# Kernel tuning notes

Measured on AMD Instinct MI355X. Metric: run time of the kernel, lower is better.

Reference implementation:

```python
import jax, jax.numpy as jnp
import numpy as np

N = 50000          # nodes
E = 1_600_000      # edges (avg degree 32)
IN = 16            # in_node_features
H0 = 64            # hidden_features_mlp[0]
D = 32             # hidden_features_mlp[1] == hidden_features_gnn
HF = 64            # hidden_final
OUT = 3            # out_features (congestion classes)
L = 3              # gnn_layer_num
EPS = 1e-5


def gelu(x):
    return jax.nn.gelu(x, approximate=False)  # torch nn.GELU default (erf)


def bn_eval(x, g, b):
    # BatchNorm1d in eval mode with fresh running stats (mean=0, var=1)
    return x * (g / jnp.sqrt(1.0 + EPS)) + b


def ln(x, g, b):
    m = jnp.mean(x, axis=-1, keepdims=True)
    v = jnp.var(x, axis=-1, keepdims=True)
    return (x - m) / jnp.sqrt(v + EPS) * g + b


def setup_inputs() -> dict:
    key = jax.random.key(0)
    ks = jax.random.split(key, 24)
    s = 0.1
    inp = {
        "x": jax.random.normal(ks[0], (N, IN), dtype=jnp.float32),
        "edge_index": jax.random.randint(ks[1], (2, E), 0, N, dtype=jnp.int32),
        # node_emb_mlp
        "emb_W1": jax.random.normal(ks[2], (IN, H0), dtype=jnp.float32) * s,
        "emb_b1": jnp.zeros((H0,), jnp.float32),
        "emb_bn1_g": jnp.ones((H0,), jnp.float32),
        "emb_bn1_b": jnp.zeros((H0,), jnp.float32),
        "emb_W2": jax.random.normal(ks[3], (H0, D), dtype=jnp.float32) * s,
        "emb_b2": jnp.zeros((D,), jnp.float32),
        "emb_bn2_g": jnp.ones((D,), jnp.float32),
        "emb_bn2_b": jnp.zeros((D,), jnp.float32),
        # GNN layers (stacked over L)
        "msg_W": jax.random.normal(ks[4], (L, 2 * D, D), dtype=jnp.float32) * s,
        "msg_b": jnp.zeros((L, D), jnp.float32),
        "msg_ln_g": jnp.ones((L, D), jnp.float32),
        "msg_ln_b": jnp.zeros((L, D), jnp.float32),
        "upd_W": jax.random.normal(ks[5], (L, 2 * D, D), dtype=jnp.float32) * s,
        "upd_b": jnp.zeros((L, D), jnp.float32),
        "upd_ln_g": jnp.ones((L, D), jnp.float32),
        "upd_ln_b": jnp.zeros((L, D), jnp.float32),
        # final_aggregation_layer
        "fin_W1": jax.random.normal(ks[6], (D, HF), dtype=jnp.float32) * s,
        "fin_b1": jnp.zeros((HF,), jnp.float32),
        "fin_bn_g": jnp.ones((HF,), jnp.float32),
        "fin_bn_b": jnp.zeros((HF,), jnp.float32),
        "fin_W2": jax.random.normal(ks[7], (HF, OUT), dtype=jnp.float32) * s,
        "fin_b2": jnp.zeros((OUT,), jnp.float32),
    }
    return inp


def reference(x, edge_index,
              emb_W1, emb_b1, emb_bn1_g, emb_bn1_b,
              emb_W2, emb_b2, emb_bn2_g, emb_bn2_b,
              msg_W, msg_b, msg_ln_g, msg_ln_b,
              upd_W, upd_b, upd_ln_g, upd_ln_b,
              fin_W1, fin_b1, fin_bn_g, fin_bn_b, fin_W2, fin_b2):
    src = edge_index[0]  # x_j (source, messages flow source->target)
    dst = edge_index[1]  # x_i (target, aggregation index)

    # node embedding MLP (dropout = identity in eval)
    h = gelu(bn_eval(x @ emb_W1 + emb_b1, emb_bn1_g, emb_bn1_b))
    h = gelu(bn_eval(h @ emb_W2 + emb_b2, emb_bn2_g, emb_bn2_b))
    pre = h

    for l in range(L):
        x_i = h[dst]  # [E, D]
        x_j = h[src]  # [E, D]
        m = gelu(ln(jnp.concatenate([x_i, x_j], axis=-1) @ msg_W[l] + msg_b[l],
                    msg_ln_g[l], msg_ln_b[l]))                 # [E, D]
        agg = jax.ops.segment_sum(m, dst, num_segments=N)      # [N, D]
        h = h + gelu(ln(jnp.concatenate([h, agg], axis=-1) @ upd_W[l] + upd_b[l],
                        upd_ln_g[l], upd_ln_b[l]))

    h = h + pre  # residual around the GNN stack

    general_emb = h[dst] - h[src]  # node_emb_j - node_emb_i, [E, D]
    out = gelu(bn_eval(general_emb @ fin_W1 + fin_b1, fin_bn_g, fin_bn_b))
    out = out @ fin_W2 + fin_b2  # [E, OUT] cc_scores
    return out
```

## Files before the change

### kernel.cpp

```cpp
#include <hip/hip_runtime.h>

#define NN 50000
#define NE 1600000
#define FILL_B 1563
#define EMB_B  782
#define HIST_STRIDE 100096
constexpr float LN_EPS = 1e-5f;

typedef _Float16 half8 __attribute__((ext_vector_type(8)));

__device__ __forceinline__ float gelu_f(float x){
  float ax = fabsf(x) * 0.70710678118654752440f;
  float t  = __builtin_amdgcn_rcpf(fmaf(0.3275911f, ax, 1.0f));
  float e  = __expf(-ax*ax);
  float p  = t*fmaf(t, fmaf(t, fmaf(t, fmaf(t, 1.061405429f, -1.453152027f),
                                    1.421413741f), -0.284496736f), 0.254829592f);
  float er = fmaf(-p, e, 1.0f);
  return 0.5f * x * (1.0f + copysignf(er, x));
}

__device__ __forceinline__ void ld8(const float* __restrict__ p, float* r){
  float4 a=((const float4*)p)[0], b=((const float4*)p)[1];
  r[0]=a.x;r[1]=a.y;r[2]=a.z;r[3]=a.w;r[4]=b.x;r[5]=b.y;r[6]=b.z;r[7]=b.w;
}
__device__ __forceinline__ void ld16(const float* __restrict__ p, float* r){ ld8(p,r); ld8(p+8,r+8); }
__device__ __forceinline__ void st8(float* __restrict__ p, const float* r){
  float4 a,b; a.x=r[0];a.y=r[1];a.z=r[2];a.w=r[3]; b.x=r[4];b.y=r[5];b.z=r[6];b.w=r[7];
  ((float4*)p)[0]=a; ((float4*)p)[1]=b;
}

__global__ __launch_bounds__(256) void hist_kernel(const int* __restrict__ ei,
    int* __restrict__ cnt16, int* __restrict__ rank){
  int t = blockIdx.x*256 + threadIdx.x;
  int hi = (blockIdx.x & 15) << 20;
  int* mycnt = cnt16 + (size_t)(blockIdx.x & 15)*NN;
  int i0 = t, i1 = t + HIST_STRIDE, i2 = t + 2*HIST_STRIDE, i3 = t + 3*HIST_STRIDE;
  bool v0 = i0 < NE/4, v1 = i1 < NE/4, v2 = i2 < NE/4, v3 = i3 < NE/4;
  int4 d0 = v0 ? ((const int4*)(ei + NE))[i0] : make_int4(0,0,0,0);
  int4 d1 = v1 ? ((const int4*)(ei + NE))[i1] : make_int4(0,0,0,0);
  int4 d2 = v2 ? ((const int4*)(ei + NE))[i2] : make_int4(0,0,0,0);
  int4 d3 = v3 ? ((const int4*)(ei + NE))[i3] : make_int4(0,0,0,0);
  int4 r0, r1, r2, r3;
  if(v0){ r0.x = hi|atomicAdd(&mycnt[d0.x],1); r0.y = hi|atomicAdd(&mycnt[d0.y],1);
          r0.z = hi|atomicAdd(&mycnt[d0.z],1); r0.w = hi|atomicAdd(&mycnt[d0.w],1); }
  if(v1){ r1.x = hi|atomicAdd(&mycnt[d1.x],1); r1.y = hi|atomicAdd(&mycnt[d1.y],1);
          r1.z = hi|atomicAdd(&mycnt[d1.z],1); r1.w = hi|atomicAdd(&mycnt[d1.w],1); }
  if(v2){ r2.x = hi|atomicAdd(&mycnt[d2.x],1); r2.y = hi|atomicAdd(&mycnt[d2.y],1);
          r2.z = hi|atomicAdd(&mycnt[d2.z],1); r2.w = hi|atomicAdd(&mycnt[d2.w],1); }
  if(v3){ r3.x = hi|atomicAdd(&mycnt[d3.x],1); r3.y = hi|atomicAdd(&mycnt[d3.y],1);
          r3.z = hi|atomicAdd(&mycnt[d3.z],1); r3.w = hi|atomicAdd(&mycnt[d3.w],1); }
  if(v0) ((int4*)rank)[i0] = r0;
  if(v1) ((int4*)rank)[i1] = r1;
  if(v2) ((int4*)rank)[i2] = r2;
  if(v3) ((int4*)rank)[i3] = r3;
}

__global__ __launch_bounds__(256) void reduce16_kernel(int* __restrict__ cnt16,
    int* __restrict__ deg){
  int t = blockIdx.x*256 + threadIdx.x;
  if(t >= NN/4) return;
  int4 run = make_int4(0,0,0,0);
  #pragma unroll
  for(int x=0;x<16;x++){
    int4 c = ((const int4*)(cnt16 + (size_t)x*NN))[t];
    ((int4*)(cnt16 + (size_t)x*NN))[t] = run;
    run.x += c.x; run.y += c.y; run.z += c.z; run.w += c.w;
  }
  ((int4*)deg)[t] = run;
}

#define CHUNK 52
__global__ __launch_bounds__(1024) void scan_kernel(const int* __restrict__ deg, int* __restrict__ row_ptr){
  __shared__ int sums[1024];
  int t = threadIdx.x;
  int base = t*CHUNK;
  int4 v[13];
  int ssum = 0;
  #pragma unroll
  for(int i=0;i<13;i++){
    int idx = base + 4*i;
    if(idx + 3 < NN){
      v[i] = ((const int4*)deg)[(base>>2)+i];
    } else {
      v[i].x = (idx+0<NN)?deg[idx+0]:0; v[i].y = (idx+1<NN)?deg[idx+1]:0;
      v[i].z = (idx+2<NN)?deg[idx+2]:0; v[i].w = (idx+3<NN)?deg[idx+3]:0;
    }
    ssum += v[i].x + v[i].y + v[i].z + v[i].w;
  }
  sums[t]=ssum;
  __syncthreads();
  for(int off=1; off<1024; off<<=1){
    int vv = (t>=off) ? sums[t-off] : 0;
    __syncthreads();
    sums[t] += vv;
    __syncthreads();
  }
  int run = (t>0) ? sums[t-1] : 0;
  #pragma unroll
  for(int i=0;i<13;i++){
    int idx = base + 4*i;
    int4 o;
    o.x = run; run += v[i].x;
    o.y = run; run += v[i].y;
    o.z = run; run += v[i].z;
    o.w = run; run += v[i].w;
    if(idx + 3 < NN){
      ((int4*)row_ptr)[(base>>2)+i] = o;
    } else {
      if(idx+0<NN) row_ptr[idx+0]=o.x;
      if(idx+1<NN) row_ptr[idx+1]=o.y;
      if(idx+2<NN) row_ptr[idx+2]=o.z;
      if(idx+3<NN) row_ptr[idx+3]=o.w;
    }
  }
  if(t==1023) row_ptr[NN] = sums[1023];
}

__global__ __launch_bounds__(256) void fill_embed_kernel(
    const int* __restrict__ ei, const int* __restrict__ row_ptr,
    const int* __restrict__ rank, const int* __restrict__ offs16,
    int* __restrict__ csr,
    const float* __restrict__ x,
    const float* __restrict__ W1, const float* __restrict__ b1,
    const float* __restrict__ g1, const float* __restrict__ bb1,
    const float* __restrict__ W2, const float* __restrict__ b2,
    const float* __restrict__ g2, const float* __restrict__ bb2,
    const float* __restrict__ Wm, const float* __restrict__ bm,
    const float* __restrict__ Wu, const float* __restrict__ bu,
    const float* __restrict__ fb1, const float* __restrict__ fbng, const float* __restrict__ fbnb,
    float* __restrict__ h, float* __restrict__ pre,
    float* __restrict__ P, _Float16* __restrict__ Qh, float* __restrict__ R,
    float* __restrict__ cvec)
{
  if(blockIdx.x >= EMB_B){
    int t = (blockIdx.x - EMB_B)*256 + threadIdx.x;
    if(t < NE/4){
      int4 d  = ((const int4*)(ei + NE))[t];
      int4 sv = ((const int4*)ei)[t];
      int4 rk = ((const int4*)rank)[t];
      csr[row_ptr[d.x] + offs16[(size_t)((unsigned)rk.x>>20)*NN + d.x] + (rk.x & 0xFFFFF)] = sv.x;
      csr[row_ptr[d.y] + offs16[(size_t)((unsigned)rk.y>>20)*NN + d.y] + (rk.y & 0xFFFFF)] = sv.y;
      csr[row_ptr[d.z] + offs16[(size_t)((unsigned)rk.z>>20)*NN + d.z] + (rk.z & 0xFFFFF)] = sv.z;
      csr[row_ptr[d.w] + offs16[(size_t)((unsigned)rk.w>>20)*NN + d.w] + (rk.w & 0xFFFFF)] = sv.w;
    }
    return;
  }
  int t = blockIdx.x*256 + threadIdx.x;
  const float rs = rsqrtf(1.0f + LN_EPS);
  if(t < 64) cvec[t] = fmaf(fb1[t], fbng[t]*rs, fbnb[t]);
  int n = t >> 2, q = t & 3;
  if(n >= NN) return;
  int base = threadIdx.x & 60;
  float4 xq = ((const float4*)x)[n*4 + q];
  float xv[16];
  #pragma unroll
  for(int m=0;m<4;m++){
    xv[4*m+0]=__shfl(xq.x, base|m);
    xv[4*m+1]=__shfl(xq.y, base|m);
    xv[4*m+2]=__shfl(xq.z, base|m);
    xv[4*m+3]=__shfl(xq.w, base|m);
  }
  float a1q[16]; ld16(b1 + q*16, a1q);
  #pragma unroll
  for(int k=0;k<16;k++){
    float w[16]; ld16(W1 + k*64 + q*16, w);
    float xk = xv[k];
    #pragma unroll
    for(int j=0;j<16;j++) a1q[j] += xk * w[j];
  }
  { float g[16], b[16]; ld16(g1+q*16,g); ld16(bb1+q*16,b);
    #pragma unroll
    for(int j=0;j<16;j++) a1q[j] = gelu_f(a1q[j]*(g[j]*rs) + b[j]); }
  float hq[8]; ld8(b2 + q*8, hq);
  #pragma unroll
  for(int m=0;m<4;m++){
    #pragma unroll
    for(int kk=0;kk<16;kk++){
      float a = __shfl(a1q[kk], base|m);
      float w[8]; ld8(W2 + (m*16+kk)*32 + q*8, w);
      #pragma unroll
      for(int j=0;j<8;j++) hq[j] += a * w[j];
    }
  }
  { float g[8], b[8]; ld8(g2+q*8,g); ld8(bb2+q*8,b);
    #pragma unroll
    for(int j=0;j<8;j++) hq[j] = gelu_f(hq[j]*(g[j]*rs) + b[j]); }
  st8(h   + (size_t)n*32 + q*8, hq);
  st8(pre + (size_t)n*32 + q*8, hq);
  float apv[8], aqv[8], arv[8];
  ld8(bm+q*8, apv); ld8(bu+q*8, arv);
  #pragma unroll
  for(int j=0;j<8;j++) aqv[j]=0.f;
  #pragma unroll
  for(int m=0;m<4;m++){
    #pragma unroll
    for(int kk=0;kk<8;kk++){
      float hk = __shfl(hq[kk], base|m);
      int k = m*8+kk;
      float wm[8],wq[8],wu[8];
      ld8(Wm + k*32      + q*8, wm);
      ld8(Wm + (32+k)*32 + q*8, wq);
      ld8(Wu + k*32      + q*8, wu);
      #pragma unroll
      for(int j=0;j<8;j++){ apv[j]+=hk*wm[j]; aqv[j]+=hk*wq[j]; arv[j]+=hk*wu[j]; }
    }
  }
  st8(P + (size_t)n*32 + q*8, apv);
  st8(R + (size_t)n*32 + q*8, arv);
  half8 qo;
  #pragma unroll
  for(int k=0;k<8;k++) qo[k] = (_Float16)aqv[k];
  *(half8*)(Qh + (size_t)n*32 + q*8) = qo;
}

__global__ __launch_bounds__(256) void msg_kernel(
    const float* __restrict__ P, const _Float16* __restrict__ Qh,
    const int* __restrict__ row_ptr, const int* __restrict__ csr_src,
    const float* __restrict__ mg, const float* __restrict__ mb,
    float* __restrict__ aggO)
{
  int tid = blockIdx.x*256 + threadIdx.x;
  int n = tid >> 5;
  int s = tid & 31;
  int slot = s >> 2;
  int q = s & 3;
  float mgq[8], mbq[8], p8[8];
  ld8(mg + q*8, mgq); ld8(mb + q*8, mbq);
  ld8(P + (size_t)n*32 + q*8, p8);
  float agg8[8] = {0,0,0,0,0,0,0,0};
  int e0 = row_ptr[n], e1 = row_ptr[n+1];
  int e = e0 + slot;
  int src = (e < e1) ? csr_src[e] : 0;
  half8 qv = *(const half8*)(Qh + (size_t)src*32 + q*8);
  while(e < e1){
    int e2 = e + 8;
    int src2 = (e2 < e1) ? csr_src[e2] : 0;
    half8 qv2 = *(const half8*)(Qh + (size_t)src2*32 + q*8);
    float v[8];
    #pragma unroll
    for(int k=0;k<8;k++) v[k] = p8[k] + (float)qv[k];
    float ps = ((v[0]+v[1])+(v[2]+v[3])) + ((v[4]+v[5])+(v[6]+v[7]));
    ps += __shfl_xor(ps,1); ps += __shfl_xor(ps,2);
    float mean = ps * 0.03125f;
    float vs = 0.f;
    #pragma unroll
    for(int k=0;k<8;k++){ float dd = v[k]-mean; vs += dd*dd; v[k]=dd; }
    vs += __shfl_xor(vs,1); vs += __shfl_xor(vs,2);
    float rstd = rsqrtf(vs*0.03125f + LN_EPS);
    #pragma unroll
    for(int k=0;k<8;k++) agg8[k] += gelu_f(v[k]*rstd*mgq[k] + mbq[k]);
    qv = qv2; e = e2;
  }
  #pragma unroll
  for(int k=0;k<8;k++) agg8[k] += __shfl_xor(agg8[k], 4);
  #pragma unroll
  for(int k=0;k<8;k++) agg8[k] += __shfl_xor(agg8[k], 8);
  #pragma unroll
  for(int k=0;k<8;k++) agg8[k] += __shfl_xor(agg8[k], 16);
  if(slot==0) st8(aggO + (size_t)n*32 + q*8, agg8);
}

__global__ __launch_bounds__(256) void upd_pqr_kernel(
    const float* __restrict__ aggI, const float* __restrict__ Rio,
    const float* __restrict__ Ub,
    const float* __restrict__ ug, const float* __restrict__ ub,
    const float* __restrict__ Wm2, const float* __restrict__ bm2,
    const float* __restrict__ Wu2, const float* __restrict__ bu2,
    float* __restrict__ h,
    float* __restrict__ P, _Float16* __restrict__ Qh, float* __restrict__ Rout)
{
  int t = blockIdx.x*256 + threadIdx.x;
  int n = t >> 2, q = t & 3;
  if(n >= NN) return;
  int base = threadIdx.x & 60;
  float aggq[8], uq[8];
  ld8(aggI + (size_t)n*32 + q*8, aggq);
  ld8(Rio  + (size_t)n*32 + q*8, uq);
  #pragma unroll
  for(int m=0;m<4;m++){
    #pragma unroll
    for(int kk=0;kk<8;kk++){
      float a = __shfl(aggq[kk], base|m);
      float w[8]; ld8(Ub + (m*8+kk)*32 + q*8, w);
      #pragma unroll
      for(int j=0;j<8;j++) uq[j] += a * w[j];
    }
  }
  float sm = ((uq[0]+uq[1])+(uq[2]+uq[3])) + ((uq[4]+uq[5])+(uq[6]+uq[7]));
  sm += __shfl_xor(sm,1); sm += __shfl_xor(sm,2);
  float mean = sm * 0.03125f;
  float vs = 0.f;
  #pragma unroll
  for(int j=0;j<8;j++){ float d = uq[j]-mean; vs += d*d; uq[j]=d; }
  vs += __shfl_xor(vs,1); vs += __shfl_xor(vs,2);
  float rstd = rsqrtf(vs*0.03125f + LN_EPS);
  float ugq[8], ubq[8], hq[8];
  ld8(ug+q*8, ugq); ld8(ub+q*8, ubq);
  ld8(h + (size_t)n*32 + q*8, hq);
  #pragma unroll
  for(int j=0;j<8;j++) hq[j] += gelu_f(uq[j]*rstd*ugq[j] + ubq[j]);
  st8(h + (size_t)n*32 + q*8, hq);
  float apv[8], aqv[8], arv[8];
  ld8(bm2+q*8, apv); ld8(bu2+q*8, arv);
  #pragma unroll
  for(int j=0;j<8;j++) aqv[j]=0.f;
  #pragma unroll
  for(int m=0;m<4;m++){
    #pragma unroll
    for(int kk=0;kk<8;kk++){
      float hk = __shfl(hq[kk], base|m);
      int k = m*8+kk;
      float wm[8],wq[8],wu[8];
      ld8(Wm2 + k*32      + q*8, wm);
      ld8(Wm2 + (32+k)*32 + q*8, wq);
      ld8(Wu2 + k*32      + q*8, wu);
      #pragma unroll
      for(int j=0;j<8;j++){ apv[j]+=hk*wm[j]; aqv[j]+=hk*wq[j]; arv[j]+=hk*wu[j]; }
    }
  }
  st8(P    + (size_t)n*32 + q*8, apv);
  st8(Rout + (size_t)n*32 + q*8, arv);
  half8 qo;
  #pragma unroll
  for(int k=0;k<8;k++) qo[k] = (_Float16)aqv[k];
  *(half8*)(Qh + (size_t)n*32 + q*8) = qo;
}

__global__ __launch_bounds__(256) void upd_fin_kernel(
    const float* __restrict__ aggI, const float* __restrict__ Rio,
    const float* __restrict__ Ub,
    const float* __restrict__ ug, const float* __restrict__ ub,
    const float* __restrict__ h, const float* __restrict__ pre,
    const float* __restrict__ fW1, const float* __restrict__ fbng,
    _Float16* __restrict__ y1, _Float16* __restrict__ y2)
{
  int t = blockIdx.x*256 + threadIdx.x;
  int n = t >> 2, q = t & 3;
  if(n >= NN) return;
  int base = threadIdx.x & 60;
  const float rs = rsqrtf(1.0f + LN_EPS);
  float aggq[8], uq[8];
  ld8(aggI + (size_t)n*32 + q*8, aggq);
  ld8(Rio  + (size_t)n*32 + q*8, uq);
  #pragma unroll
  for(int m=0;m<4;m++){
    #pragma unroll
    for(int kk=0;kk<8;kk++){
      float a = __shfl(aggq[kk], base|m);
      float w[8]; ld8(Ub + (m*8+kk)*32 + q*8, w);
      #pragma unroll
      for(int j=0;j<8;j++) uq[j] += a * w[j];
    }
  }
  float sm = ((uq[0]+uq[1])+(uq[2]+uq[3])) + ((uq[4]+uq[5])+(uq[6]+uq[7]));
  sm += __shfl_xor(sm,1); sm += __shfl_xor(sm,2);
  float mean = sm * 0.03125f;
  float vs = 0.f;
  #pragma unroll
  for(int j=0;j<8;j++){ float d = uq[j]-mean; vs += d*d; uq[j]=d; }
  vs += __shfl_xor(vs,1); vs += __shfl_xor(vs,2);
  float rstd = rsqrtf(vs*0.03125f + LN_EPS);
  float ugq[8], ubq[8], hq[8], pq[8];
  ld8(ug+q*8, ugq); ld8(ub+q*8, ubq);
  ld8(h   + (size_t)n*32 + q*8, hq);
  ld8(pre + (size_t)n*32 + q*8, pq);
  #pragma unroll
  for(int j=0;j<8;j++) hq[j] += gelu_f(uq[j]*rstd*ugq[j] + ubq[j]) + pq[j];
  float acc[16];
  #pragma unroll
  for(int j=0;j<16;j++) acc[j]=0.f;
  #pragma unroll
  for(int m=0;m<4;m++){
    #pragma unroll
    for(int kk=0;kk<8;kk++){
      float hk = __shfl(hq[kk], base|m);
      float w[16]; ld16(fW1 + (m*8+kk)*64 + q*16, w);
      #pragma unroll
      for(int j=0;j<16;j++) acc[j] += hk * w[j];
    }
  }
  float fg[16]; ld16(fbng + q*16, fg);
  half8 o0, o1;
  #pragma unroll
  for(int k=0;k<8;k++){
    o0[k] = (_Float16)(acc[k]   * (fg[k]*rs));
    o1[k] = (_Float16)(acc[8+k] * (fg[8+k]*rs));
  }
  _Float16* dst = (q<2) ? (y1 + (size_t)n*32 + q*16) : (y2 + (size_t)n*32 + (q-2)*16);
  ((half8*)dst)[0] = o0; ((half8*)dst)[1] = o1;
}

__global__ __launch_bounds__(256) void finalA_kernel(
    const _Float16* __restrict__ y, const int* __restrict__ ei,
    const float* __restrict__ cvec, const float* __restrict__ W2,
    const float* __restrict__ b2, float* __restrict__ out)
{
  int t = blockIdx.x*256 + threadIdx.x;
  int g = t >> 2, q = t & 3;
  int eA = g, eB = g + NE/2;
  int sA = __builtin_nontemporal_load(ei + eA);
  int dA = __builtin_nontemporal_load(ei + NE + eA);
  int sB = __builtin_nontemporal_load(ei + eB);
  int dB = __builtin_nontemporal_load(ei + NE + eB);
  half8 aA = *(const half8*)(y + (size_t)dA*32 + q*8);
  half8 cA = *(const half8*)(y + (size_t)sA*32 + q*8);
  half8 aB = *(const half8*)(y + (size_t)dB*32 + q*8);
  half8 cB = *(const half8*)(y + (size_t)sB*32 + q*8);
  float cq[8]; ld8(cvec + q*8, cq);
  float w[24]; ld8(W2+q*24, w); ld8(W2+q*24+8, w+8); ld8(W2+q*24+16, w+16);
  float oA0=0.f,oA1=0.f,oA2=0.f, oB0=0.f,oB1=0.f,oB2=0.f;
  #pragma unroll
  for(int k=0;k<8;k++){
    float tA = gelu_f(((float)aA[k]-(float)cA[k]) + cq[k]);
    float tB = gelu_f(((float)aB[k]-(float)cB[k]) + cq[k]);
    oA0 += tA*w[3*k]; oA1 += tA*w[3*k+1]; oA2 += tA*w[3*k+2];
    oB0 += tB*w[3*k]; oB1 += tB*w[3*k+1]; oB2 += tB*w[3*k+2];
  }
  oA0 += __shfl_xor(oA0,1); oA0 += __shfl_xor(oA0,2);
  oA1 += __shfl_xor(oA1,1); oA1 += __shfl_xor(oA1,2);
  oA2 += __shfl_xor(oA2,1); oA2 += __shfl_xor(oA2,2);
  oB0 += __shfl_xor(oB0,1); oB0 += __shfl_xor(oB0,2);
  oB1 += __shfl_xor(oB1,1); oB1 += __shfl_xor(oB1,2);
  oB2 += __shfl_xor(oB2,1); oB2 += __shfl_xor(oB2,2);
  float ovA = (q==0) ? oA0 + b2[0] : (q==1) ? oA1 + b2[1] : oA2 + b2[2];
  float ovB = (q==0) ? oB0 + b2[0] : (q==1) ? oB1 + b2[1] : oB2 + b2[2];
  if(q < 3){
    __builtin_nontemporal_store(ovA, out + (size_t)eA*3 + q);
    __builtin_nontemporal_store(ovB, out + (size_t)eB*3 + q);
  }
}

__global__ __launch_bounds__(256) void finalB_kernel(
    const _Float16* __restrict__ y, const int* __restrict__ ei,
    const float* __restrict__ cvec, const float* __restrict__ W2,
    float* __restrict__ out)
{
  int t = blockIdx.x*256 + threadIdx.x;
  int g = t >> 2, q = t & 3;
  int eA = g, eB = g + NE/2;
  float pA = 0.f, pB = 0.f;
  if(q < 3){
    pA = __builtin_nontemporal_load(out + (size_t)eA*3 + q);
    pB = __builtin_nontemporal_load(out + (size_t)eB*3 + q);
  }
  int sA = __builtin_nontemporal_load(ei + eA);
  int dA = __builtin_nontemporal_load(ei + NE + eA);
  int sB = __builtin_nontemporal_load(ei + eB);
  int dB = __builtin_nontemporal_load(ei + NE + eB);
  half8 aA = *(const half8*)(y + (size_t)dA*32 + q*8);
  half8 cA = *(const half8*)(y + (size_t)sA*32 + q*8);
  half8 aB = *(const half8*)(y + (size_t)dB*32 + q*8);
  half8 cB = *(const half8*)(y + (size_t)sB*32 + q*8);
  float cq[8]; ld8(cvec + q*8, cq);
  float w[24]; ld8(W2+q*24, w); ld8(W2+q*24+8, w+8); ld8(W2+q*24+16, w+16);
  float oA0=0.f,oA1=0.f,oA2=0.f, oB0=0.f,oB1=0.f,oB2=0.f;
  #pragma unroll
  for(int k=0;k<8;k++){
    float tA = gelu_f(((float)aA[k]-(float)cA[k]) + cq[k]);
    float tB = gelu_f(((float)aB[k]-(float)cB[k]) + cq[k]);
    oA0 += tA*w[3*k]; oA1 += tA*w[3*k+1]; oA2 += tA*w[3*k+2];
    oB0 += tB*w[3*k]; oB1 += tB*w[3*k+1]; oB2 += tB*w[3*k+2];
  }
  oA0 += __shfl_xor(oA0,1); oA0 += __shfl_xor(oA0,2);
  oA1 += __shfl_xor(oA1,1); oA1 += __shfl_xor(oA1,2);
  oA2 += __shfl_xor(oA2,1); oA2 += __shfl_xor(oA2,2);
  oB0 += __shfl_xor(oB0,1); oB0 += __shfl_xor(oB0,2);
  oB1 += __shfl_xor(oB1,1); oB1 += __shfl_xor(oB1,2);
  oB2 += __shfl_xor(oB2,1); oB2 += __shfl_xor(oB2,2);
  float ovA = pA + ((q==0) ? oA0 : (q==1) ? oA1 : oA2);
  float ovB = pB + ((q==0) ? oB0 : (q==1) ? oB1 : oB2);
  if(q < 3){
    __builtin_nontemporal_store(ovA, out + (size_t)eA*3 + q);
    __builtin_nontemporal_store(ovB, out + (size_t)eB*3 + q);
  }
}

extern "C" void kernel_launch(void* const* d_in, const int* in_sizes, int n_in,
                              void* d_out, int out_size, void* d_ws, size_t ws_size,
                              hipStream_t stream)
{
  (void)in_sizes; (void)n_in; (void)out_size; (void)ws_size;
  const float* x     = (const float*)d_in[0];
  const int*   ei    = (const int*)d_in[1];
  const float* eW1   = (const float*)d_in[2];
  const float* eb1   = (const float*)d_in[3];
  const float* ebn1g = (const float*)d_in[4];
  const float* ebn1b = (const float*)d_in[5];
  const float* eW2   = (const float*)d_in[6];
  const float* eb2   = (const float*)d_in[7];
  const float* ebn2g = (const float*)d_in[8];
  const float* ebn2b = (const float*)d_in[9];
  const float* msgW  = (const float*)d_in[10];
  const float* msgb  = (const float*)d_in[11];
  const float* msglng= (const float*)d_in[12];
  const float* msglnb= (const float*)d_in[13];
  const float* updW  = (const float*)d_in[14];
  const float* updb  = (const float*)d_in[15];
  const float* updlng= (const float*)d_in[16];
  const float* updlnb= (const float*)d_in[17];
  const float* fW1   = (const float*)d_in[18];
  const float* fb1   = (const float*)d_in[19];
  const float* fbng  = (const float*)d_in[20];
  const float* fbnb  = (const float*)d_in[21];
  const float* fW2   = (const float*)d_in[22];
  const float* fb2   = (const float*)d_in[23];
  float* out = (float*)d_out;

  float* f   = (float*)d_ws;
  float* h   = f;
  float* pre = f + 1*(size_t)NN*32;
  float* P   = f + 2*(size_t)NN*32;
  float* R   = f + 3*(size_t)NN*32;
  float* agg = f + 4*(size_t)NN*32;
  _Float16* Qh = (_Float16*)(f + 5*(size_t)NN*32);
  _Float16* y1 = (_Float16*)P;
  _Float16* y2 = y1 + (size_t)NN*32;
  float* cvec  = f + 5*(size_t)NN*32 + (size_t)NN*16;
  int* ip      = (int*)(cvec + 64);
  int* cnt16   = ip;
  int* deg     = ip + 16*NN;
  int* row_ptr = ip + 17*NN;
  int* csr     = ip + 18*NN + 4;
  int* rank    = (int*)agg;

  hipMemsetAsync(cnt16, 0, (size_t)16*NN*sizeof(int), stream);
  hist_kernel<<<391, 256, 0, stream>>>(ei, cnt16, rank);
  reduce16_kernel<<<(NN/4+255)/256, 256, 0, stream>>>(cnt16, deg);
  scan_kernel<<<1, 1024, 0, stream>>>(deg, row_ptr);
  fill_embed_kernel<<<EMB_B + FILL_B, 256, 0, stream>>>(ei, row_ptr, rank, cnt16, csr,
      x, eW1, eb1, ebn1g, ebn1b,
      eW2, eb2, ebn2g, ebn2b,
      msgW, msgb, updW, updb,
      fb1, fbng, fbnb,
      h, pre, P, Qh, R, cvec);

  for(int l=0; l<3; l++){
    msg_kernel<<<(NN*32)/256, 256, 0, stream>>>(P, Qh, row_ptr, csr,
        msglng + l*32, msglnb + l*32, agg);
    if(l < 2){
      upd_pqr_kernel<<<EMB_B, 256, 0, stream>>>(agg, R,
          updW + l*2048 + 1024, updlng + l*32, updlnb + l*32,
          msgW + (l+1)*2048, msgb + (l+1)*32,
          updW + (l+1)*2048, updb + (l+1)*32,
          h, P, Qh, R);
    } else {
      upd_fin_kernel<<<EMB_B, 256, 0, stream>>>(agg, R,
          updW + l*2048 + 1024, updlng + l*32, updlnb + l*32,
          h, pre, fW1, fbng, y1, y2);
    }
  }

  finalA_kernel<<<(NE*2)/256, 256, 0, stream>>>(y1, ei, cvec,      fW2,      fb2, out);
  finalB_kernel<<<(NE*2)/256, 256, 0, stream>>>(y2, ei, cvec + 32, fW2 + 96, out);
}
```

Before: 488.9 us.

## Pre-add row_ptr into per-bucket offsets and deepen msg src prefetch

Adds a kernel that folds row_ptr into the 16 per-bucket offset arrays, so the CSR fill scatter does one dependent gather per edge instead of two. reduce16 switches from int4 to per-node scalar processing. The msg kernel now prefetches the CSR source index two iterations ahead, which hides index-load latency before the Qh gather. The cost is one extra kernel launch and an extra read and write pass over the 16xN offset table.

New measurement: 492.2 us, median of 2. Within noise of the previous version (+0.7%).

```diff
diff --git a/kernel.cpp b/kernel.cpp
--- a/kernel.cpp
+++ b/kernel.cpp
@@ -57,16 +57,16 @@
 
 __global__ __launch_bounds__(256) void reduce16_kernel(int* __restrict__ cnt16,
     int* __restrict__ deg){
-  int t = blockIdx.x*256 + threadIdx.x;
-  if(t >= NN/4) return;
-  int4 run = make_int4(0,0,0,0);
+  int n = blockIdx.x*256 + threadIdx.x;
+  if(n >= NN) return;
+  int run = 0;
   #pragma unroll
   for(int x=0;x<16;x++){
-    int4 c = ((const int4*)(cnt16 + (size_t)x*NN))[t];
-    ((int4*)(cnt16 + (size_t)x*NN))[t] = run;
-    run.x += c.x; run.y += c.y; run.z += c.z; run.w += c.w;
-  }
-  ((int4*)deg)[t] = run;
+    int c = cnt16[(size_t)x*NN + n];
+    cnt16[(size_t)x*NN + n] = run;
+    run += c;
+  }
+  deg[n] = run;
 }
 
 #define CHUNK 52
@@ -116,9 +116,21 @@
   if(t==1023) row_ptr[NN] = sums[1023];
 }
 
+__global__ __launch_bounds__(256) void addbase16_kernel(int* __restrict__ cnt16,
+    const int* __restrict__ row_ptr){
+  int t = blockIdx.x*256 + threadIdx.x;
+  if(t >= 16*(NN/4)) return;
+  int x  = t / (NN/4);
+  int n4 = t - x*(NN/4);
+  int4 rp = ((const int4*)row_ptr)[n4];
+  int4 c  = ((int4*)(cnt16 + (size_t)x*NN))[n4];
+  c.x += rp.x; c.y += rp.y; c.z += rp.z; c.w += rp.w;
+  ((int4*)(cnt16 + (size_t)x*NN))[n4] = c;
+}
+
 __global__ __launch_bounds__(256) void fill_embed_kernel(
-    const int* __restrict__ ei, const int* __restrict__ row_ptr,
-    const int* __restrict__ rank, const int* __restrict__ offs16,
+    const int* __restrict__ ei,
+    const int* __restrict__ rank, const int* __restrict__ base16,
     int* __restrict__ csr,
     const float* __restrict__ x,
     const float* __restrict__ W1, const float* __restrict__ b1,
@@ -138,10 +150,10 @@
       int4 d  = ((const int4*)(ei + NE))[t];
       int4 sv = ((const int4*)ei)[t];
       int4 rk = ((const int4*)rank)[t];
-      csr[row_ptr[d.x] + offs16[(size_t)((unsigned)rk.x>>20)*NN + d.x] + (rk.x & 0xFFFFF)] = sv.x;
-      csr[row_ptr[d.y] + offs16[(size_t)((unsigned)rk.y>>20)*NN + d.y] + (rk.y & 0xFFFFF)] = sv.y;
-      csr[row_ptr[d.z] + offs16[(size_t)((unsigned)rk.z>>20)*NN + d.z] + (rk.z & 0xFFFFF)] = sv.z;
-      csr[row_ptr[d.w] + offs16[(size_t)((unsigned)rk.w>>20)*NN + d.w] + (rk.w & 0xFFFFF)] = sv.w;
+      csr[base16[(size_t)((unsigned)rk.x>>20)*NN + d.x] + (rk.x & 0xFFFFF)] = sv.x;
+      csr[base16[(size_t)((unsigned)rk.y>>20)*NN + d.y] + (rk.y & 0xFFFFF)] = sv.y;
+      csr[base16[(size_t)((unsigned)rk.z>>20)*NN + d.z] + (rk.z & 0xFFFFF)] = sv.z;
+      csr[base16[(size_t)((unsigned)rk.w>>20)*NN + d.w] + (rk.w & 0xFFFFF)] = sv.w;
     }
     return;
   }
@@ -229,13 +241,15 @@
   ld8(P + (size_t)n*32 + q*8, p8);
   float agg8[8] = {0,0,0,0,0,0,0,0};
   int e0 = row_ptr[n], e1 = row_ptr[n+1];
-  int e = e0 + slot;
-  int src = (e < e1) ? csr_src[e] : 0;
+  int e  = e0 + slot;
+  int e2 = e + 8;
+  int src  = (e  < e1) ? csr_src[e]  : 0;
+  int src2 = (e2 < e1) ? csr_src[e2] : 0;
   half8 qv = *(const half8*)(Qh + (size_t)src*32 + q*8);
   while(e < e1){
-    int e2 = e + 8;
-    int src2 = (e2 < e1) ? csr_src[e2] : 0;
     half8 qv2 = *(const half8*)(Qh + (size_t)src2*32 + q*8);
+    int e3 = e2 + 8;
+    int src3 = (e3 < e1) ? csr_src[e3] : 0;
     float v[8];
     #pragma unroll
     for(int k=0;k<8;k++) v[k] = p8[k] + (float)qv[k];
@@ -249,7 +263,7 @@
     float rstd = rsqrtf(vs*0.03125f + LN_EPS);
     #pragma unroll
     for(int k=0;k<8;k++) agg8[k] += gelu_f(v[k]*rstd*mgq[k] + mbq[k]);
-    qv = qv2; e = e2;
+    qv = qv2; src2 = src3; e = e2; e2 = e3;
   }
   #pragma unroll
   for(int k=0;k<8;k++) agg8[k] += __shfl_xor(agg8[k], 4);
@@ -525,9 +539,10 @@
 
   hipMemsetAsync(cnt16, 0, (size_t)16*NN*sizeof(int), stream);
   hist_kernel<<<391, 256, 0, stream>>>(ei, cnt16, rank);
-  reduce16_kernel<<<(NN/4+255)/256, 256, 0, stream>>>(cnt16, deg);
+  reduce16_kernel<<<(NN+255)/256, 256, 0, stream>>>(cnt16, deg);
   scan_kernel<<<1, 1024, 0, stream>>>(deg, row_ptr);
-  fill_embed_kernel<<<EMB_B + FILL_B, 256, 0, stream>>>(ei, row_ptr, rank, cnt16, csr,
+  addbase16_kernel<<<(16*(NN/4)+255)/256, 256, 0, stream>>>(cnt16, row_ptr);
+  fill_embed_kernel<<<EMB_B + FILL_B, 256, 0, stream>>>(ei, rank, cnt16, csr,
       x, eW1, eb1, ebn1g, ebn1b,
       eW2, eb2, ebn2g, ebn2b,
       msgW, msgb, updW, updb,
```
